# Optimization experiments

Hardware: AMD Instinct MI355X
Metric: run time of the kernel (lower is better)

Reference implementation:

```python
import jax, jax.numpy as jnp
import numpy as np

N_EMBD = 768
N_HEAD = 8
HEAD_DIM = N_EMBD // N_HEAD


def setup_inputs() -> dict:
    key = jax.random.key(0)
    k1, k2, k3 = jax.random.split(key, 3)
    B, T, C = 8, 1024, N_EMBD
    x = jax.random.normal(k1, (B, T, C), dtype=jnp.float32)
    # nn.Linear(C, 3C, bias=False): store as [C, 3C] so y = x @ W
    W_attn = jax.random.normal(k2, (C, 3 * C), dtype=jnp.float32) * (1.0 / np.sqrt(C))
    W_proj = jax.random.normal(k3, (C, C), dtype=jnp.float32) * (1.0 / np.sqrt(C))
    return {"x": x, "W_attn": W_attn, "W_proj": W_proj}


def reference(x, W_attn, W_proj):
    B, T, C = x.shape
    qkv = x @ W_attn                      # [B,T,3C]
    q, k, v = jnp.split(qkv, 3, axis=2)
    # [B,T,C] -> [B,H,T,D]
    def heads(t):
        return t.reshape(B, T, N_HEAD, HEAD_DIM).transpose(0, 2, 1, 3)
    q, k, v = heads(q), heads(k), heads(v)
    scale = 1.0 / np.sqrt(HEAD_DIM)
    att = jnp.einsum('bhtd,bhsd->bhts', q, k) * scale  # [B,H,T,T]
    causal = jnp.tril(jnp.ones((T, T), dtype=bool))
    att = jnp.where(causal[None, None], att, -jnp.inf)
    att = jax.nn.softmax(att, axis=-1)
    y = jnp.einsum('bhts,bhsd->bhtd', att, v)          # [B,H,T,D]
    y = y.transpose(0, 2, 1, 3).reshape(B, T, C)
    return y @ W_proj
```

## Files before the change

kernel.cpp:

```cpp
#include <hip/hip_runtime.h>
#include <stdint.h>

#define Bz 8
#define Tz 1024
#define Cz 768
#define Hz 8
#define Dz 96
#define BHz 64
#define Kz 768

typedef __bf16 bf16x8 __attribute__((ext_vector_type(8)));
typedef unsigned short u16x8 __attribute__((ext_vector_type(8)));
typedef float f32x4 __attribute__((ext_vector_type(4)));

__device__ __forceinline__ unsigned short f2bf(float f) {
  union { float f; unsigned int u; } v; v.f = f;
  unsigned int u = v.u;
  return (unsigned short)((u + 0x7fffu + ((u >> 16) & 1u)) >> 16);
}

__device__ __forceinline__ unsigned int cvtpk(float a, float b) {
  unsigned int r;
  asm("v_cvt_pk_bf16_f32 %0, %1, %2" : "=v"(r) : "v"(a), "v"(b));
  return r;
}

#if defined(__has_builtin)
#if __has_builtin(__builtin_amdgcn_exp2f)
#define EXP2(x) __builtin_amdgcn_exp2f(x)
#endif
#endif
#ifndef EXP2
#define EXP2(x) __expf((x) * 0.6931471805599453f)
#endif

typedef const __attribute__((address_space(1))) void* gas_ptr;
typedef __attribute__((address_space(3))) void* las_ptr;
__device__ __forceinline__ void gl16(const void* g, void* l) {
  __builtin_amdgcn_global_load_lds((gas_ptr)g, (las_ptr)l, 16, 0, 0);
}

__global__ __launch_bounds__(256) void prep(const float* __restrict__ x,
                                            unsigned short* __restrict__ xb,
                                            const float* __restrict__ Wa,
                                            unsigned short* __restrict__ Wat,
                                            const float* __restrict__ Wp,
                                            unsigned short* __restrict__ Wpt) {
  __shared__ unsigned short t[64][72];
  const int bid = blockIdx.x;
  const int tid = threadIdx.x;
  if (bid < 6144) {
    int i = (bid * 256 + tid) * 4;
    float4 v = *(const float4*)(x + i);
    union { unsigned short s[4]; uint2 u; } o;
    o.s[0] = f2bf(v.x); o.s[1] = f2bf(v.y); o.s[2] = f2bf(v.z); o.s[3] = f2bf(v.w);
    *(uint2*)(xb + i) = o.u;
    return;
  }
  const float* in; unsigned short* out; int R, Cc, bx, by;
  if (bid < 6576) { int q = bid - 6144; in = Wa; out = Wat; R = 768; Cc = 2304; bx = (q % 36) * 64; by = (q / 36) * 64; }
  else            { int q = bid - 6576; in = Wp; out = Wpt; R = 768; Cc = 768;  bx = (q % 12) * 64; by = (q / 12) * 64; }
#pragma unroll
  for (int i = 0; i < 16; i++) {
    int idx = tid + i * 256;
    int r = idx >> 6, c = idx & 63;
    t[c][r] = f2bf(in[(by + r) * Cc + bx + c]);
  }
  __syncthreads();
#pragma unroll
  for (int i = 0; i < 16; i++) {
    int idx = tid + i * 256;
    int r = idx >> 6, c = idx & 63;
    out[(bx + r) * R + by + c] = t[r][c];
  }
}

template <int MODE>
__global__ __launch_bounds__(256)
void gemm128(const unsigned short* __restrict__ A,
             const unsigned short* __restrict__ Bt,
             unsigned short* __restrict__ obf,
             float* __restrict__ of32) {
  __shared__ unsigned short Asm[128 * 64];
  __shared__ unsigned short Bsm[128 * 64];
  const int tid = threadIdx.x;
  const int wave = tid >> 6, lane = tid & 63;
  const int quad = lane >> 4, l16 = lane & 15;
  const int bm = blockIdx.x, bn = blockIdx.y;
  const int wm = (wave >> 1) * 64, wn = (wave & 1) * 64;

  f32x4 zero = {0.f, 0.f, 0.f, 0.f};
  f32x4 acc[4][4];
#pragma unroll
  for (int i = 0; i < 4; i++)
#pragma unroll
    for (int j = 0; j < 4; j++) acc[i][j] = zero;

  const int srow = lane >> 3;
  const int sch = (lane & 7) ^ srow;
  const unsigned short* Ag[4];
  const unsigned short* Bg[4];
#pragma unroll
  for (int g = 0; g < 4; g++) {
    Ag[g] = A + (size_t)(bm * 128 + g * 32 + wave * 8 + srow) * Kz + sch * 8;
    Bg[g] = Bt + (size_t)(bn * 128 + g * 32 + wave * 8 + srow) * Kz + sch * 8;
  }

  for (int k0 = 0; k0 < Kz; k0 += 64) {
    __syncthreads();
#pragma unroll
    for (int g = 0; g < 4; g++) {
      gl16(Ag[g] + k0, &Asm[(g * 32 + wave * 8) * 64]);
      gl16(Bg[g] + k0, &Bsm[(g * 32 + wave * 8) * 64]);
    }
    __syncthreads();
#pragma unroll
    for (int kk = 0; kk < 2; kk++) {
      const int rc = (((kk * 4 + quad) ^ (l16 & 7)) << 3);
      bf16x8 af[4], bfr[4];
#pragma unroll
      for (int mi = 0; mi < 4; mi++)
        af[mi] = *(const bf16x8*)&Asm[(wm + mi * 16 + l16) * 64 + rc];
#pragma unroll
      for (int ni = 0; ni < 4; ni++)
        bfr[ni] = *(const bf16x8*)&Bsm[(wn + ni * 16 + l16) * 64 + rc];
#pragma unroll
      for (int mi = 0; mi < 4; mi++)
#pragma unroll
        for (int ni = 0; ni < 4; ni++)
          acc[mi][ni] = __builtin_amdgcn_mfma_f32_16x16x32_bf16(af[mi], bfr[ni], acc[mi][ni], 0, 0, 0);
    }
  }

#pragma unroll
  for (int mi = 0; mi < 4; mi++) {
    int row = bm * 128 + wm + mi * 16 + quad * 4;
    if (MODE == 0) {
      int b = row >> 10;
      int t = row & 1023;
#pragma unroll
      for (int ni = 0; ni < 4; ni++) {
        int col = bn * 128 + wn + ni * 16 + l16;
        int which = col / 768;
        int cc = col - which * 768;
        int h = cc / 96;
        int d = cc - h * 96;
        if (which == 2) {
          int base = ((2 * 64 + b * 8 + h) * 96 + d) * 1024 + t;
          union { unsigned short s[4]; uint2 u; } o;
#pragma unroll
          for (int r = 0; r < 4; r++) o.s[r] = f2bf(acc[mi][ni][r]);
          *(uint2*)(obf + base) = o.u;
        } else {
          int base = ((which * 64 + b * 8 + h) * 1024 + t) * 96 + d;
#pragma unroll
          for (int r = 0; r < 4; r++) obf[base + r * 96] = f2bf(acc[mi][ni][r]);
        }
      }
    } else {
#pragma unroll
      for (int ni = 0; ni < 4; ni++) {
        int col = bn * 128 + wn + ni * 16 + l16;
#pragma unroll
        for (int r = 0; r < 4; r++) of32[(row + r) * 768 + col] = acc[mi][ni][r];
      }
    }
  }
}

__global__ __launch_bounds__(256, 4)
void attn(const unsigned short* __restrict__ qkv, unsigned short* __restrict__ y) {
  const int bh = blockIdx.x;
  const int by = blockIdx.y;
  const int q0 = (15 - by) * 64;
  const int tid = threadIdx.x;
  const int wave = tid >> 6, lane = tid & 63;
  const int quad = lane >> 4, l16 = lane & 15;
  const int qw0 = q0 + wave * 16;
  const int b = bh >> 3, h = bh & 7;

  const unsigned short* Qh = qkv + bh * Tz * Dz;
  const unsigned short* Kh = qkv + (BHz + bh) * Tz * Dz;
  const unsigned short* Vt = qkv + 2 * BHz * Tz * Dz + bh * Dz * Tz;

  __shared__ unsigned short Vsm[96 * 128];

  bf16x8 aq[3];
#pragma unroll
  for (int kd = 0; kd < 3; kd++)
    aq[kd] = *(const bf16x8*)(Qh + (qw0 + l16) * Dz + kd * 32 + quad * 8);

  f32x4 zero = {0.f, 0.f, 0.f, 0.f};
  f32x4 acc_o[6];
#pragma unroll
  for (int i = 0; i < 6; i++) acc_o[i] = zero;
  const float NEG = -__builtin_inff();
  float mrow = NEG, lrow = 0.f;
  const float cs = 0.14724538519872735f;
  const int t_abs = qw0 + l16;

  const int vrow = wave * 24 + (lane >> 4);
  const int vch = lane & 15;

  const int s_last = (q0 >> 7) << 7;
  for (int s0 = 0; s0 <= s_last; s0 += 128) {
    __syncthreads();
#pragma unroll
    for (int g = 0; g < 6; g++) {
      const int row = vrow + g * 4;
      gl16(Vt + row * Tz + s0 + ((vch ^ (row & 7)) << 3),
           &Vsm[(wave * 24 + g * 4) * 128]);
    }

    const int srem = qw0 + 15 - s0;
    const int nlim = min(7, srem >> 4);
    const int klim = min(3, srem >> 5);

    f32x4 sacc[8];
#pragma unroll
    for (int ni = 0; ni < 8; ni++) {
      if (ni <= nlim) {
        sacc[ni] = zero;
#pragma unroll
        for (int kd = 0; kd < 3; kd++) {
          bf16x8 bk = *(const bf16x8*)(Kh + (s0 + ni * 16 + l16) * Dz + kd * 32 + quad * 8);
          sacc[ni] = __builtin_amdgcn_mfma_f32_16x16x32_bf16(bk, aq[kd], sacc[ni], 0, 0, 0);
        }
      }
    }

    float rmx[4] = {NEG, NEG, NEG, NEG};
#pragma unroll
    for (int ni = 0; ni < 8; ni++) {
      if (ni <= nlim) {
        if (s0 + ni * 16 + 15 > qw0) {
          const int s_base = s0 + ni * 16 + quad * 4;
#pragma unroll
          for (int r = 0; r < 4; r++)
            if (s_base + r > t_abs) sacc[ni][r] = NEG;
        }
#pragma unroll
        for (int r = 0; r < 4; r++) rmx[r] = fmaxf(rmx[r], sacc[ni][r]);
      }
    }
    float rmax = fmaxf(fmaxf(rmx[0], rmx[1]), fmaxf(rmx[2], rmx[3]));
    rmax = fmaxf(rmax, __shfl_xor(rmax, 16));
    rmax = fmaxf(rmax, __shfl_xor(rmax, 32));

    int ok = (rmax <= mrow + 54.0f) ? 1 : 0;
    if (!__all(ok)) {
      float mnew = fmaxf(mrow, rmax);
      float alpha = EXP2((mrow - mnew) * cs);
      mrow = mnew;
      lrow *= alpha;
      float av[4];
#pragma unroll
      for (int r = 0; r < 4; r++) av[r] = __shfl(alpha, quad * 4 + r);
#pragma unroll
      for (int di = 0; di < 6; di++)
#pragma unroll
        for (int r = 0; r < 4; r++) acc_o[di][r] *= av[r];
    }

    const float nmc = -mrow * cs;
    float rs[4] = {0.f, 0.f, 0.f, 0.f};
    unsigned int pk[8][2];
#pragma unroll
    for (int ni = 0; ni < 8; ni++) {
      if (ni <= nlim) {
        float p0 = EXP2(fmaf(sacc[ni][0], cs, nmc));
        float p1 = EXP2(fmaf(sacc[ni][1], cs, nmc));
        float p2 = EXP2(fmaf(sacc[ni][2], cs, nmc));
        float p3 = EXP2(fmaf(sacc[ni][3], cs, nmc));
        rs[0] += p0; rs[1] += p1; rs[2] += p2; rs[3] += p3;
        pk[ni][0] = cvtpk(p0, p1);
        pk[ni][1] = cvtpk(p2, p3);
      } else {
        pk[ni][0] = 0u; pk[ni][1] = 0u;
      }
    }
    lrow += (rs[0] + rs[1]) + (rs[2] + rs[3]);

    __syncthreads();

#pragma unroll
    for (int kc = 0; kc < 4; kc++) {
      if (kc <= klim) {
        const unsigned int a0 = pk[2 * kc][0], a1 = pk[2 * kc][1];
        const unsigned int b0 = pk[2 * kc + 1][0], b1 = pk[2 * kc + 1][1];
        const unsigned int s0w = (quad < 2) ? b0 : a0;
        const unsigned int s1w = (quad < 2) ? b1 : a1;
        const unsigned int u0 = (unsigned int)__shfl_xor((int)s0w, 32);
        const unsigned int u1 = (unsigned int)__shfl_xor((int)s1w, 32);
        const unsigned int t0w = (quad == 0 || quad == 3) ? u0 : ((quad == 1) ? a0 : b0);
        const unsigned int t1w = (quad == 0 || quad == 3) ? u1 : ((quad == 1) ? a1 : b1);
        const unsigned int r0 = (unsigned int)__shfl_xor((int)t0w, 16);
        const unsigned int r1 = (unsigned int)__shfl_xor((int)t1w, 16);
        union { unsigned int w[4]; bf16x8 v; } ap;
        ap.w[0] = (quad == 0) ? a0 : ((quad == 2) ? u0 : r0);
        ap.w[1] = (quad == 0) ? a1 : ((quad == 2) ? u1 : r1);
        ap.w[2] = (quad == 0) ? r0 : ((quad == 1) ? u0 : ((quad == 2) ? r0 : b0));
        ap.w[3] = (quad == 0) ? r1 : ((quad == 1) ? u1 : ((quad == 2) ? r1 : b1));
#pragma unroll
        for (int di = 0; di < 6; di++) {
          bf16x8 bv = *(const bf16x8*)&Vsm[(di * 16 + l16) * 128 +
                                           (((kc * 4 + quad) ^ (l16 & 7)) << 3)];
          acc_o[di] = __builtin_amdgcn_mfma_f32_16x16x32_bf16(ap.v, bv, acc_o[di], 0, 0, 0);
        }
      }
    }
  }

  lrow += __shfl_xor(lrow, 16);
  lrow += __shfl_xor(lrow, 32);
  float linv = 1.f / lrow;
  float lv[4];
#pragma unroll
  for (int r = 0; r < 4; r++) lv[r] = __shfl(linv, quad * 4 + r);
#pragma unroll
  for (int r = 0; r < 4; r++) {
    int t = qw0 + quad * 4 + r;
#pragma unroll
    for (int di = 0; di < 6; di++) {
      int d = di * 16 + l16;
      y[(b * Tz + t) * Cz + h * Dz + d] = f2bf(acc_o[di][r] * lv[r]);
    }
  }
}

#define OFF_XB   0u
#define OFF_WAT  12582912u
#define OFF_WPT  16121856u
#define OFF_QKV  17301504u
#define OFF_Y    55050240u

extern "C" void kernel_launch(void* const* d_in, const int* in_sizes, int n_in,
                              void* d_out, int out_size, void* d_ws, size_t ws_size,
                              hipStream_t stream) {
  const float* x  = (const float*)d_in[0];
  const float* Wa = (const float*)d_in[1];
  const float* Wp = (const float*)d_in[2];
  float* out = (float*)d_out;
  uint8_t* ws = (uint8_t*)d_ws;
  unsigned short* xb  = (unsigned short*)(ws + OFF_XB);
  unsigned short* Wat = (unsigned short*)(ws + OFF_WAT);
  unsigned short* Wpt = (unsigned short*)(ws + OFF_WPT);
  unsigned short* qkv = (unsigned short*)(ws + OFF_QKV);
  unsigned short* y   = (unsigned short*)(ws + OFF_Y);

  prep<<<6720, 256, 0, stream>>>(x, xb, Wa, Wat, Wp, Wpt);
  gemm128<0><<<dim3(64, 18), 256, 0, stream>>>(xb, Wat, qkv, nullptr);
  attn<<<dim3(64, 16), 256, 0, stream>>>(qkv, y);
  gemm128<1><<<dim3(64, 6), 256, 0, stream>>>(y, Wpt, nullptr, out);
}
```

Baseline: 200.6 us.

## Double-buffer GEMM LDS tiles with BK=32 to overlap loads and MFMA

The 128x128 bf16 GEMM now keeps two 128x32 shared-memory buffers per operand. It issues the next k-slice's global-to-LDS loads before computing on the current one, with one barrier per iteration instead of two. This is meant to hide global load latency behind the MFMA work. In exchange the k-step halves, so the loop runs twice as many iterations. The swizzle is also redone for 32-wide rows, which could introduce LDS bank conflicts or correctness risk if the pattern is wrong.

```diff
diff --git a/kernel.cpp b/kernel.cpp
--- a/kernel.cpp
+++ b/kernel.cpp
@@ -81,8 +81,8 @@
              const unsigned short* __restrict__ Bt,
              unsigned short* __restrict__ obf,
              float* __restrict__ of32) {
-  __shared__ unsigned short Asm[128 * 64];
-  __shared__ unsigned short Bsm[128 * 64];
+  __shared__ unsigned short Asm[2][128 * 32];
+  __shared__ unsigned short Bsm[2][128 * 32];
   const int tid = threadIdx.x;
   const int wave = tid >> 6, lane = tid & 63;
   const int quad = lane >> 4, l16 = lane & 15;
@@ -96,40 +96,43 @@
 #pragma unroll
     for (int j = 0; j < 4; j++) acc[i][j] = zero;
 
-  const int srow = lane >> 3;
-  const int sch = (lane & 7) ^ srow;
-  const unsigned short* Ag[4];
-  const unsigned short* Bg[4];
-#pragma unroll
-  for (int g = 0; g < 4; g++) {
-    Ag[g] = A + (size_t)(bm * 128 + g * 32 + wave * 8 + srow) * Kz + sch * 8;
-    Bg[g] = Bt + (size_t)(bn * 128 + g * 32 + wave * 8 + srow) * Kz + sch * 8;
-  }
-
-  for (int k0 = 0; k0 < Kz; k0 += 64) {
+  const int sch = (lane & 3) ^ ((lane >> 3) & 3);
+  const unsigned short* Agp = A + (size_t)(bm * 128 + wave * 16 + (lane >> 2)) * Kz + sch * 8;
+  const unsigned short* Bgp = Bt + (size_t)(bn * 128 + wave * 16 + (lane >> 2)) * Kz + sch * 8;
+  const int ldst = (wave * 16) * 32;
+
+#pragma unroll
+  for (int g = 0; g < 2; g++) {
+    gl16(Agp + g * 64 * Kz, &Asm[0][g * 2048 + ldst]);
+    gl16(Bgp + g * 64 * Kz, &Bsm[0][g * 2048 + ldst]);
+  }
+  __syncthreads();
+
+  const int rc = (quad ^ ((l16 >> 1) & 3)) << 3;
+  int cur = 0;
+  for (int t = 0; t < Kz / 32; t++) {
+    if (t + 1 < Kz / 32) {
+      const int kn = (t + 1) * 32;
+#pragma unroll
+      for (int g = 0; g < 2; g++) {
+        gl16(Agp + g * 64 * Kz + kn, &Asm[cur ^ 1][g * 2048 + ldst]);
+        gl16(Bgp + g * 64 * Kz + kn, &Bsm[cur ^ 1][g * 2048 + ldst]);
+      }
+    }
+    bf16x8 af[4], bfr[4];
+#pragma unroll
+    for (int mi = 0; mi < 4; mi++)
+      af[mi] = *(const bf16x8*)&Asm[cur][(wm + mi * 16 + l16) * 32 + rc];
+#pragma unroll
+    for (int ni = 0; ni < 4; ni++)
+      bfr[ni] = *(const bf16x8*)&Bsm[cur][(wn + ni * 16 + l16) * 32 + rc];
+#pragma unroll
+    for (int mi = 0; mi < 4; mi++)
+#pragma unroll
+      for (int ni = 0; ni < 4; ni++)
+        acc[mi][ni] = __builtin_amdgcn_mfma_f32_16x16x32_bf16(af[mi], bfr[ni], acc[mi][ni], 0, 0, 0);
     __syncthreads();
-#pragma unroll
-    for (int g = 0; g < 4; g++) {
-      gl16(Ag[g] + k0, &Asm[(g * 32 + wave * 8) * 64]);
-      gl16(Bg[g] + k0, &Bsm[(g * 32 + wave * 8) * 64]);
-    }
-    __syncthreads();
-#pragma unroll
-    for (int kk = 0; kk < 2; kk++) {
-      const int rc = (((kk * 4 + quad) ^ (l16 & 7)) << 3);
-      bf16x8 af[4], bfr[4];
-#pragma unroll
-      for (int mi = 0; mi < 4; mi++)
-        af[mi] = *(const bf16x8*)&Asm[(wm + mi * 16 + l16) * 64 + rc];
-#pragma unroll
-      for (int ni = 0; ni < 4; ni++)
-        bfr[ni] = *(const bf16x8*)&Bsm[(wn + ni * 16 + l16) * 64 + rc];
-#pragma unroll
-      for (int mi = 0; mi < 4; mi++)
-#pragma unroll
-        for (int ni = 0; ni < 4; ni++)
-          acc[mi][ni] = __builtin_amdgcn_mfma_f32_16x16x32_bf16(af[mi], bfr[ni], acc[mi][ni], 0, 0, 0);
-    }
+    cur ^= 1;
   }
 
 #pragma unroll
```

Measured after the change: 206.7 us. +3.0%, slower.
